# Kernel optimization log

Measured on AMD Instinct MI355X. Metric: run time of the kernel, lower is better.

Reference implementation:

```python
import jax, jax.numpy as jnp
import numpy as np

B, S, D, H, L = 16, 1024, 128, 8, 3
DFF = 4 * D  # 512
DH = D // H  # 16
NUM_CLASSES = 6


def layernorm(x, g, b, eps):
    mu = jnp.mean(x, axis=-1, keepdims=True)
    var = jnp.mean(jnp.square(x - mu), axis=-1, keepdims=True)
    return g * (x - mu) / jnp.sqrt(var + eps) + b


def setup_inputs() -> dict:
    key = jax.random.key(0)
    ks = jax.random.split(key, 16)
    sc = 0.05
    inp = {
        'x': jax.random.normal(ks[0], (B, S, D), dtype=jnp.float32),
        'Wq': jax.random.normal(ks[1], (L, D, D), dtype=jnp.float32) * sc,
        'bq': jnp.zeros((L, D), dtype=jnp.float32),
        'Wk': jax.random.normal(ks[2], (L, D, D), dtype=jnp.float32) * sc,
        'bk': jnp.zeros((L, D), dtype=jnp.float32),
        'Wv': jax.random.normal(ks[3], (L, D, D), dtype=jnp.float32) * sc,
        'bv': jnp.zeros((L, D), dtype=jnp.float32),
        'ln1_g': jnp.ones((L, D), dtype=jnp.float32),
        'ln1_b': jnp.zeros((L, D), dtype=jnp.float32),
        'W1': jax.random.normal(ks[4], (L, D, DFF), dtype=jnp.float32) * sc,
        'b1': jnp.zeros((L, DFF), dtype=jnp.float32),
        'W2': jax.random.normal(ks[5], (L, DFF, D), dtype=jnp.float32) * sc,
        'b2': jnp.zeros((L, D), dtype=jnp.float32),
        'ln2_g': jnp.ones((L, D), dtype=jnp.float32),
        'ln2_b': jnp.zeros((L, D), dtype=jnp.float32),
        'Wout': jax.random.normal(ks[6], (D, NUM_CLASSES), dtype=jnp.float32) * sc,
        'bout': jnp.zeros((NUM_CLASSES,), dtype=jnp.float32),
    }
    return inp


def reference(x, Wq, bq, Wk, bk, Wv, bv, ln1_g, ln1_b, W1, b1, W2, b2, ln2_g, ln2_b, Wout, bout):
    scale = 1.0 / jnp.sqrt(jnp.float32(DH))
    for l in range(L):
        # Q/K/V projections with ReLU activation (as in source Dense(..., relu))
        q = jax.nn.relu(jnp.einsum('bsd,de->bse', x, Wq[l]) + bq[l])
        k = jax.nn.relu(jnp.einsum('bsd,de->bse', x, Wk[l]) + bk[l])
        v = jax.nn.relu(jnp.einsum('bsd,de->bse', x, Wv[l]) + bv[l])
        # split-heads (tf.split axis=-1 / concat axis=0 == reshape to heads)
        qh = q.reshape(B, S, H, DH)
        kh = k.reshape(B, S, H, DH)
        vh = v.reshape(B, S, H, DH)
        scores = jnp.einsum('bqhd,bkhd->bhqk', qh, kh) * scale  # [B,H,S,S]
        attn = jax.nn.softmax(scores, axis=-1)
        o = jnp.einsum('bhqk,bkhd->bqhd', attn, vh).reshape(B, S, D)
        x = layernorm(o + x, ln1_g[l], ln1_b[l], 1e-8)
        # pointwise FFN (Conv1D kernel_size=1 == dense over last dim)
        h = jax.nn.relu(jnp.einsum('bsd,df->bsf', x, W1[l]) + b1[l])
        f = jnp.einsum('bsf,fd->bsd', h, W2[l]) + b2[l]
        x = layernorm(f + x, ln2_g[l], ln2_b[l], 1e-6)
    return jnp.einsum('bsd,dc->bsc', x, Wout) + bout
```

## Files before the change

kernel.cpp:

```cpp
#include <hip/hip_runtime.h>
#include <math.h>

#define Bq 16
#define Sq 1024
#define Dq 128
#define Hq 8
#define DHq 16
#define DFFq 512
#define Lq 3
#define NCLS 6
#define NROWS (Bq * Sq)
#define NX ((size_t)NROWS * Dq)

typedef __attribute__((ext_vector_type(8))) short    bf16x8;
typedef __attribute__((ext_vector_type(4))) float    f32x4;
typedef __attribute__((ext_vector_type(4))) _Float16 f16x4;
typedef __attribute__((ext_vector_type(8))) _Float16 f16x8;

__device__ inline ushort f32_to_bf16(float f) {
    union { float f; unsigned u; } v; v.f = f;
    unsigned r = v.u + 0x7fffu + ((v.u >> 16) & 1u);
    return (ushort)(r >> 16);
}

__global__ __launch_bounds__(256) void prep_kernel(
    const float* __restrict__ Wqp, const float* __restrict__ Wkp,
    const float* __restrict__ Wvp, const float* __restrict__ W1p,
    const float* __restrict__ W2p, const float* __restrict__ xp,
    ushort* __restrict__ wbf, ushort* __restrict__ xbf)
{
    const int gid = blockIdx.x * 256 + threadIdx.x;
    if (gid < 147456) {
        const int w   = gid / 49152;
        const int rem = gid - w * 49152;
        const int l   = rem >> 14;
        const int idx = rem & 16383;
        const int k   = idx >> 7;
        const int n   = idx & 127;
        const float* src = (w == 0) ? Wqp : (w == 1) ? Wkp : Wvp;
        const float scl = (w == 0) ? 0.25f : 1.0f;
        wbf[(size_t)(w * 3 + l) * 16384 + n * 128 + k] =
            f32_to_bf16(src[(size_t)l * 16384 + k * 128 + n] * scl);
    } else if (gid < 344064) {
        const int g   = gid - 147456;
        const int l   = g >> 16;
        const int idx = g & 65535;
        const int k   = idx >> 9;
        const int n   = idx & 511;
        wbf[147456 + (size_t)l * 65536 + n * 128 + k] =
            f32_to_bf16(W1p[(size_t)l * 65536 + k * 512 + n]);
    } else if (gid < 540672) {
        const int g   = gid - 344064;
        const int l   = g >> 16;
        const int idx = g & 65535;
        const int k   = idx >> 7;
        const int n   = idx & 127;
        wbf[344064 + (size_t)l * 65536 + n * 512 + k] =
            f32_to_bf16(W2p[(size_t)l * 65536 + k * 128 + n]);
    } else {
        const int g = gid - 540672;
        xbf[g] = f32_to_bf16(xp[g]);
    }
}

__global__ __launch_bounds__(256) void gemm_qkv(
    const ushort* __restrict__ A,
    const ushort* __restrict__ wq, const ushort* __restrict__ wk,
    const ushort* __restrict__ wv,
    const float* __restrict__ bqp, const float* __restrict__ bkp,
    const float* __restrict__ bvp,
    _Float16* __restrict__ qo, _Float16* __restrict__ ko,
    _Float16* __restrict__ vo)
{
    __shared__ ushort As[64 * 40];
    __shared__ ushort Bs[128 * 40];

    const int sel  = blockIdx.y;
    const ushort* Bt   = (sel == 0) ? wq : (sel == 1) ? wk : wv;
    const float*  bias = (sel == 0) ? bqp : (sel == 1) ? bkp : bvp;
    const float   bscl = (sel == 0) ? 0.25f : 1.0f;

    const int tid  = threadIdx.x;
    const int row0 = blockIdx.x * 64;
    const int wave = tid >> 6;
    const int lane = tid & 63;
    const int quad = lane >> 4;
    const int m16  = lane & 15;
    const int wm   = wave >> 1;
    const int wn   = wave & 1;

    const int sar = tid >> 2;
    const int sac = (tid & 3) * 8;

    f32x4 acc[2][4];
    #pragma unroll
    for (int i = 0; i < 2; ++i)
        #pragma unroll
        for (int j = 0; j < 4; ++j) acc[i][j] = (f32x4)0.f;

    for (int k0 = 0; k0 < 128; k0 += 32) {
        bf16x8 av = *(const bf16x8*)(A + (size_t)(row0 + sar) * 128 + k0 + sac);
        const int r1 = tid >> 2, r2 = r1 + 64;
        bf16x8 bv1 = *(const bf16x8*)(Bt + (size_t)r1 * 128 + k0 + sac);
        bf16x8 bv2 = *(const bf16x8*)(Bt + (size_t)r2 * 128 + k0 + sac);

        __syncthreads();
        *(bf16x8*)&As[sar * 40 + sac] = av;
        *(bf16x8*)&Bs[r1 * 40 + sac]  = bv1;
        *(bf16x8*)&Bs[r2 * 40 + sac]  = bv2;
        __syncthreads();

        bf16x8 af[2], bf[4];
        #pragma unroll
        for (int i = 0; i < 2; ++i)
            af[i] = *(const bf16x8*)&As[(32 * wm + 16 * i + m16) * 40 + quad * 8];
        #pragma unroll
        for (int j = 0; j < 4; ++j)
            bf[j] = *(const bf16x8*)&Bs[(64 * wn + 16 * j + m16) * 40 + quad * 8];
        #pragma unroll
        for (int i = 0; i < 2; ++i)
            #pragma unroll
            for (int j = 0; j < 4; ++j)
                acc[i][j] = __builtin_amdgcn_mfma_f32_16x16x32_bf16(af[i], bf[j], acc[i][j], 0, 0, 0);
    }

    #pragma unroll
    for (int i = 0; i < 2; ++i) {
        #pragma unroll
        for (int j = 0; j < 4; ++j) {
            const int col = 64 * wn + 16 * j + m16;
            const float bb = bias[col] * bscl;
            const int hh = col >> 4, dh = col & 15;
            #pragma unroll
            for (int r = 0; r < 4; ++r) {
                float val = fmaxf(acc[i][j][r] + bb, 0.f);
                const int gr = row0 + 32 * wm + 16 * i + quad * 4 + r;
                const int b = gr >> 10, s = gr & 1023;
                if (sel == 2) {
                    vo[(((size_t)b * Hq + hh) * DHq + dh) * Sq + s] = (_Float16)val;
                } else {
                    _Float16* outp = (sel == 0) ? qo : ko;
                    outp[(((size_t)b * Hq + hh) * Sq + s) * DHq + dh] = (_Float16)val;
                }
            }
        }
    }
}

__global__ __launch_bounds__(256) void gemm_ffn_fused(
    const float* __restrict__ o, const float* __restrict__ resid,
    const float* __restrict__ g1, const float* __restrict__ beta1,
    const ushort* __restrict__ W1t, const float* __restrict__ bias1,
    const ushort* __restrict__ W2t, const float* __restrict__ bias2,
    const float* __restrict__ g2, const float* __restrict__ beta2,
    float* __restrict__ xb, ushort* __restrict__ xbbf,
    const float* __restrict__ Wout, const float* __restrict__ bout,
    float* __restrict__ out, int last)
{
    __shared__ __align__(16) char smem[77696];
    ushort* Af   = (ushort*)smem;
    ushort* Hs   = (ushort*)(smem + 17408);
    ushort* Bs   = (ushort*)(smem + 50688);
    float*  wo_s = (float*)(smem + 50688);
    float*  vals = (float*)(smem + 60928);
    float*  mus  = (float*)(smem + 77440);
    float*  rsds = (float*)(smem + 77568);

    const int tid  = threadIdx.x;
    const int row0 = blockIdx.x * 32;
    const int wave = tid >> 6;
    const int lane = tid & 63;
    const int quad = lane >> 4;
    const int m16  = lane & 15;
    const int wm   = wave >> 1;
    const int wn   = wave & 1;
    const int sac  = (tid & 3) * 8;
    const int r1   = tid >> 2, r2 = r1 + 64;

    #pragma unroll 2
    for (int it = 0; it < 8; ++it) {
        const int rr = wave * 8 + it;
        const size_t base = (size_t)(row0 + rr) * Dq;
        float v0 = o[base + lane]      + resid[base + lane];
        float v1 = o[base + 64 + lane] + resid[base + 64 + lane];

        float s = v0 + v1;
        #pragma unroll
        for (int off = 32; off > 0; off >>= 1) s += __shfl_xor(s, off, 64);
        const float mu = s * (1.f / 128.f);
        const float d0 = v0 - mu, d1 = v1 - mu;
        float vs = d0 * d0 + d1 * d1;
        #pragma unroll
        for (int off = 32; off > 0; off >>= 1) vs += __shfl_xor(vs, off, 64);
        const float rstd = rsqrtf(vs * (1.f / 128.f) + 1e-8f);

        const float rv0 = g1[lane]      * d0 * rstd + beta1[lane];
        const float rv1 = g1[lane + 64] * d1 * rstd + beta1[lane + 64];
        Af[rr * 136 + lane]        = f32_to_bf16(rv0);
        Af[rr * 136 + 64 + lane]   = f32_to_bf16(rv1);
        vals[rr * 129 + lane]      = rv0;
        vals[rr * 129 + 64 + lane] = rv1;
    }

    for (int cc = 0; cc < 4; ++cc) {
        f32x4 acc[4];
        #pragma unroll
        for (int j = 0; j < 4; ++j) acc[j] = (f32x4)0.f;

        for (int k0 = 0; k0 < 128; k0 += 32) {
            bf16x8 bv1 = *(const bf16x8*)(W1t + (size_t)(cc * 128 + r1) * 128 + k0 + sac);
            bf16x8 bv2 = *(const bf16x8*)(W1t + (size_t)(cc * 128 + r2) * 128 + k0 + sac);

            __syncthreads();
            *(bf16x8*)&Bs[r1 * 40 + sac] = bv1;
            *(bf16x8*)&Bs[r2 * 40 + sac] = bv2;
            __syncthreads();

            const bf16x8 af = *(const bf16x8*)&Af[(16 * wm + m16) * 136 + k0 + quad * 8];
            bf16x8 bf[4];
            #pragma unroll
            for (int j = 0; j < 4; ++j)
                bf[j] = *(const bf16x8*)&Bs[(64 * wn + 16 * j + m16) * 40 + quad * 8];
            #pragma unroll
            for (int j = 0; j < 4; ++j)
                acc[j] = __builtin_amdgcn_mfma_f32_16x16x32_bf16(af, bf[j], acc[j], 0, 0, 0);
        }

        #pragma unroll
        for (int j = 0; j < 4; ++j) {
            const int col = cc * 128 + 64 * wn + 16 * j + m16;
            const float bb = bias1[col];
            #pragma unroll
            for (int r = 0; r < 4; ++r) {
                const int row = 16 * wm + quad * 4 + r;
                Hs[row * 520 + col] = f32_to_bf16(fmaxf(acc[j][r] + bb, 0.f));
            }
        }
    }

    f32x4 acc2[4];
    #pragma unroll
    for (int j = 0; j < 4; ++j) acc2[j] = (f32x4)0.f;

    for (int k0 = 0; k0 < DFFq; k0 += 32) {
        bf16x8 bv1 = *(const bf16x8*)(W2t + (size_t)r1 * DFFq + k0 + sac);
        bf16x8 bv2 = *(const bf16x8*)(W2t + (size_t)r2 * DFFq + k0 + sac);

        __syncthreads();
        *(bf16x8*)&Bs[r1 * 40 + sac] = bv1;
        *(bf16x8*)&Bs[r2 * 40 + sac] = bv2;
        __syncthreads();

        const bf16x8 af = *(const bf16x8*)&Hs[(16 * wm + m16) * 520 + k0 + quad * 8];
        bf16x8 bf[4];
        #pragma unroll
        for (int j = 0; j < 4; ++j)
            bf[j] = *(const bf16x8*)&Bs[(64 * wn + 16 * j + m16) * 40 + quad * 8];
        #pragma unroll
        for (int j = 0; j < 4; ++j)
            acc2[j] = __builtin_amdgcn_mfma_f32_16x16x32_bf16(af, bf[j], acc2[j], 0, 0, 0);
    }

    __syncthreads();

    float vreg[4][4];
    #pragma unroll
    for (int j = 0; j < 4; ++j) {
        const int col = 64 * wn + 16 * j + m16;
        const float bb = bias2[col];
        #pragma unroll
        for (int r = 0; r < 4; ++r) {
            const int row = 16 * wm + quad * 4 + r;
            float v = acc2[j][r] + bb + vals[row * 129 + col];
            vreg[j][r] = v;
            vals[row * 129 + col] = v;
        }
    }
    if (last) {
        #pragma unroll
        for (int i = 0; i < 3; ++i) wo_s[tid + i * 256] = Wout[tid + i * 256];
    }
    __syncthreads();

    if (tid < 32) {
        float s = 0.f, s2 = 0.f;
        #pragma unroll 8
        for (int c = 0; c < Dq; ++c) {
            float x = vals[tid * 129 + c];
            s += x; s2 = fmaf(x, x, s2);
        }
        const float mu  = s * (1.f / 128.f);
        const float var = s2 * (1.f / 128.f) - mu * mu;
        mus[tid]  = mu;
        rsds[tid] = rsqrtf(var + 1e-6f);
    }
    __syncthreads();

    if (!last) {
        #pragma unroll
        for (int j = 0; j < 4; ++j) {
            const int col = 64 * wn + 16 * j + m16;
            #pragma unroll
            for (int r = 0; r < 4; ++r) {
                const int row = 16 * wm + quad * 4 + r;
                const float rn = g2[col] * (vreg[j][r] - mus[row]) * rsds[row] + beta2[col];
                const size_t idx = (size_t)(row0 + row) * Dq + col;
                xb[idx]   = rn;
                xbbf[idx] = f32_to_bf16(rn);
            }
        }
    } else {
        #pragma unroll
        for (int j = 0; j < 4; ++j) {
            const int col = 64 * wn + 16 * j + m16;
            #pragma unroll
            for (int r = 0; r < 4; ++r) {
                const int row = 16 * wm + quad * 4 + r;
                vals[row * 129 + col] = g2[col] * (vreg[j][r] - mus[row]) * rsds[row] + beta2[col];
            }
        }
        __syncthreads();
        if (tid < 32 * NCLS) {
            const int row = tid / NCLS;
            const int c   = tid - row * NCLS;
            float a = bout[c];
            #pragma unroll 8
            for (int kk = 0; kk < Dq; ++kk)
                a = fmaf(vals[row * 129 + kk], wo_s[kk * NCLS + c], a);
            out[(size_t)(row0 + row) * NCLS + c] = a;
        }
    }
}

__global__ __launch_bounds__(256) void attn_mfma(
    const _Float16* __restrict__ q, const _Float16* __restrict__ k,
    const _Float16* __restrict__ vt, float* __restrict__ o)
{
    __shared__ _Float16 Ks[256 * 20];
    __shared__ _Float16 Vs[16 * 264];

    const int bh   = blockIdx.x;
    const int qc   = blockIdx.y;
    const int b    = bh >> 3;
    const int h    = bh & 7;
    const int tid  = threadIdx.x;
    const int wave = tid >> 6;
    const int lane = tid & 63;
    const int quad = lane >> 4;
    const int m16  = lane & 15;
    const int q0   = qc * 128 + wave * 32;

    const f16x4 qf0 = *(const f16x4*)(q + (((size_t)bh * Sq) + q0 + m16) * DHq + quad * 4);
    const f16x4 qf1 = *(const f16x4*)(q + (((size_t)bh * Sq) + q0 + 16 + m16) * DHq + quad * 4);

    const _Float16* kg  = k  + (size_t)bh * Sq * DHq;
    const _Float16* vtg = vt + (size_t)bh * DHq * Sq;

    f32x4 oacc0 = (f32x4)0.f, oacc1 = (f32x4)0.f;
    float lacc0 = 0.f, lacc1 = 0.f;

    const int krow = tid;
    const int vrow = tid >> 4;
    const int vcol = (tid & 15) * 16;

    for (int kb = 0; kb < 4; ++kb) {
        f16x8 ka  = *(const f16x8*)(kg + ((size_t)kb * 256 + krow) * DHq);
        f16x8 kb8 = *(const f16x8*)(kg + ((size_t)kb * 256 + krow) * DHq + 8);
        f16x8 va  = *(const f16x8*)(vtg + (size_t)vrow * Sq + kb * 256 + vcol);
        f16x8 vb  = *(const f16x8*)(vtg + (size_t)vrow * Sq + kb * 256 + vcol + 8);
        __syncthreads();
        *(f16x8*)&Ks[krow * 20 + 0] = ka;
        *(f16x8*)&Ks[krow * 20 + 8] = kb8;
        *(f16x8*)&Vs[vrow * 264 + vcol + 0] = va;
        *(f16x8*)&Vs[vrow * 264 + vcol + 8] = vb;
        __syncthreads();

        #pragma unroll 4
        for (int kt = 0; kt < 16; ++kt) {
            const f16x4 kf = *(const f16x4*)&Ks[(kt * 16 + m16) * 20 + quad * 4];
            const f16x4 vf = *(const f16x4*)&Vs[m16 * 264 + kt * 16 + quad * 4];

            f32x4 st0 = __builtin_amdgcn_mfma_f32_16x16x16f16(kf, qf0, (f32x4)0.f, 0, 0, 0);
            f32x4 st1 = __builtin_amdgcn_mfma_f32_16x16x16f16(kf, qf1, (f32x4)0.f, 0, 0, 0);

            float p00 = __expf(st0[0]);
            float p01 = __expf(st0[1]);
            float p02 = __expf(st0[2]);
            float p03 = __expf(st0[3]);
            float p10 = __expf(st1[0]);
            float p11 = __expf(st1[1]);
            float p12 = __expf(st1[2]);
            float p13 = __expf(st1[3]);
            lacc0 += (p00 + p01) + (p02 + p03);
            lacc1 += (p10 + p11) + (p12 + p13);

            f16x4 pf0, pf1;
            pf0[0] = (_Float16)p00; pf0[1] = (_Float16)p01;
            pf0[2] = (_Float16)p02; pf0[3] = (_Float16)p03;
            pf1[0] = (_Float16)p10; pf1[1] = (_Float16)p11;
            pf1[2] = (_Float16)p12; pf1[3] = (_Float16)p13;

            oacc0 = __builtin_amdgcn_mfma_f32_16x16x16f16(pf0, vf, oacc0, 0, 0, 0);
            oacc1 = __builtin_amdgcn_mfma_f32_16x16x16f16(pf1, vf, oacc1, 0, 0, 0);
        }
    }

    lacc0 += __shfl_xor(lacc0, 16, 64);
    lacc0 += __shfl_xor(lacc0, 32, 64);
    lacc1 += __shfl_xor(lacc1, 16, 64);
    lacc1 += __shfl_xor(lacc1, 32, 64);

    #pragma unroll
    for (int r = 0; r < 4; ++r) {
        const float ls0 = __shfl(lacc0, quad * 4 + r, 64);
        const float ls1 = __shfl(lacc1, quad * 4 + r, 64);
        o[((size_t)b * Sq + q0 + quad * 4 + r) * Dq + h * DHq + m16]      = oacc0[r] / ls0;
        o[((size_t)b * Sq + q0 + 16 + quad * 4 + r) * Dq + h * DHq + m16] = oacc1[r] / ls1;
    }
}

extern "C" void kernel_launch(void* const* d_in, const int* in_sizes, int n_in,
                              void* d_out, int out_size, void* d_ws, size_t ws_size,
                              hipStream_t stream)
{
    const float* x_in  = (const float*)d_in[0];
    const float* Wq    = (const float*)d_in[1];
    const float* bq    = (const float*)d_in[2];
    const float* Wk    = (const float*)d_in[3];
    const float* bk    = (const float*)d_in[4];
    const float* Wv    = (const float*)d_in[5];
    const float* bv    = (const float*)d_in[6];
    const float* ln1_g = (const float*)d_in[7];
    const float* ln1_b = (const float*)d_in[8];
    const float* W1    = (const float*)d_in[9];
    const float* b1    = (const float*)d_in[10];
    const float* W2    = (const float*)d_in[11];
    const float* b2    = (const float*)d_in[12];
    const float* ln2_g = (const float*)d_in[13];
    const float* ln2_b = (const float*)d_in[14];
    const float* Wout  = (const float*)d_in[15];
    const float* bout  = (const float*)d_in[16];
    float* out = (float*)d_out;

    float* ws = (float*)d_ws;
    _Float16* qf16 = (_Float16*)ws;
    _Float16* kf16 = (_Float16*)(ws + NX / 2);
    _Float16* vt16 = (_Float16*)(ws + NX);
    float*    xb   = ws + 9 * NX / 2;
    ushort*   xbf0 = (ushort*)(ws + 11 * NX / 2);
    ushort*   xbbf = (ushort*)(ws + 13 * NX / 2);
    ushort*   wbf  = (ushort*)(ws + 7 * NX);
    float*    obuf = ws + 8 * NX;

    prep_kernel<<<dim3(10304), dim3(256), 0, stream>>>(Wq, Wk, Wv, W1, W2, x_in, wbf, xbf0);

    const dim3 blk(256);
    const float* xcur = x_in;
    const ushort* xcur_bf = xbf0;

    for (int l = 0; l < Lq; ++l) {
        const ushort* wqt = wbf + (size_t)(0 * 3 + l) * 16384;
        const ushort* wkt = wbf + (size_t)(1 * 3 + l) * 16384;
        const ushort* wvt = wbf + (size_t)(2 * 3 + l) * 16384;
        const ushort* w1t = wbf + 147456 + (size_t)l * 65536;
        const ushort* w2t = wbf + 344064 + (size_t)l * 65536;

        gemm_qkv<<<dim3(256, 3), blk, 0, stream>>>(
            xcur_bf, wqt, wkt, wvt, bq + l * Dq, bk + l * Dq, bv + l * Dq,
            qf16, kf16, vt16);

        attn_mfma<<<dim3(Bq * Hq, 8), blk, 0, stream>>>(qf16, kf16, vt16, obuf);

        gemm_ffn_fused<<<dim3(512), blk, 0, stream>>>(
            obuf, xcur, ln1_g + l * Dq, ln1_b + l * Dq,
            w1t, b1 + l * DFFq, w2t, b2 + l * Dq,
            ln2_g + l * Dq, ln2_b + l * Dq,
            xb, xbbf, Wout, bout, out, (l == Lq - 1) ? 1 : 0);

        xcur = xb;
        xcur_bf = xbbf;
    }
}
```

Measured before the change: 278.8 us.

## Register-prefetch next tiles in GEMMs and attention; double queries per attention wave

```diff
diff --git a/kernel.cpp b/kernel.cpp
--- a/kernel.cpp
+++ b/kernel.cpp
@@ -91,6 +91,7 @@
 
     const int sar = tid >> 2;
     const int sac = (tid & 3) * 8;
+    const int r1  = tid >> 2, r2 = r1 + 64;
 
     f32x4 acc[2][4];
     #pragma unroll
@@ -98,17 +99,23 @@
         #pragma unroll
         for (int j = 0; j < 4; ++j) acc[i][j] = (f32x4)0.f;
 
-    for (int k0 = 0; k0 < 128; k0 += 32) {
-        bf16x8 av = *(const bf16x8*)(A + (size_t)(row0 + sar) * 128 + k0 + sac);
-        const int r1 = tid >> 2, r2 = r1 + 64;
-        bf16x8 bv1 = *(const bf16x8*)(Bt + (size_t)r1 * 128 + k0 + sac);
-        bf16x8 bv2 = *(const bf16x8*)(Bt + (size_t)r2 * 128 + k0 + sac);
-
+    bf16x8 av  = *(const bf16x8*)(A  + (size_t)(row0 + sar) * 128 + sac);
+    bf16x8 bv1 = *(const bf16x8*)(Bt + (size_t)r1 * 128 + sac);
+    bf16x8 bv2 = *(const bf16x8*)(Bt + (size_t)r2 * 128 + sac);
+
+    for (int kc = 0; kc < 4; ++kc) {
         __syncthreads();
         *(bf16x8*)&As[sar * 40 + sac] = av;
         *(bf16x8*)&Bs[r1 * 40 + sac]  = bv1;
         *(bf16x8*)&Bs[r2 * 40 + sac]  = bv2;
         __syncthreads();
+
+        if (kc < 3) {
+            const int k0 = (kc + 1) * 32;
+            av  = *(const bf16x8*)(A  + (size_t)(row0 + sar) * 128 + k0 + sac);
+            bv1 = *(const bf16x8*)(Bt + (size_t)r1 * 128 + k0 + sac);
+            bv2 = *(const bf16x8*)(Bt + (size_t)r2 * 128 + k0 + sac);
+        }
 
         bf16x8 af[2], bf[4];
         #pragma unroll
@@ -202,54 +209,74 @@
         vals[rr * 129 + 64 + lane] = rv1;
     }
 
-    for (int cc = 0; cc < 4; ++cc) {
-        f32x4 acc[4];
-        #pragma unroll
-        for (int j = 0; j < 4; ++j) acc[j] = (f32x4)0.f;
-
-        for (int k0 = 0; k0 < 128; k0 += 32) {
-            bf16x8 bv1 = *(const bf16x8*)(W1t + (size_t)(cc * 128 + r1) * 128 + k0 + sac);
-            bf16x8 bv2 = *(const bf16x8*)(W1t + (size_t)(cc * 128 + r2) * 128 + k0 + sac);
-
-            __syncthreads();
-            *(bf16x8*)&Bs[r1 * 40 + sac] = bv1;
-            *(bf16x8*)&Bs[r2 * 40 + sac] = bv2;
-            __syncthreads();
-
-            const bf16x8 af = *(const bf16x8*)&Af[(16 * wm + m16) * 136 + k0 + quad * 8];
-            bf16x8 bf[4];
+    bf16x8 pv1 = *(const bf16x8*)(W1t + (size_t)r1 * 128 + sac);
+    bf16x8 pv2 = *(const bf16x8*)(W1t + (size_t)r2 * 128 + sac);
+
+    f32x4 acc[4];
+    #pragma unroll
+    for (int j = 0; j < 4; ++j) acc[j] = (f32x4)0.f;
+
+    for (int idx = 0; idx < 16; ++idx) {
+        const int cc = idx >> 2;
+        const int k0 = (idx & 3) * 32;
+
+        __syncthreads();
+        *(bf16x8*)&Bs[r1 * 40 + sac] = pv1;
+        *(bf16x8*)&Bs[r2 * 40 + sac] = pv2;
+        __syncthreads();
+
+        if (idx < 15) {
+            const int n   = idx + 1;
+            const int ncc = n >> 2;
+            const int nk0 = (n & 3) * 32;
+            pv1 = *(const bf16x8*)(W1t + (size_t)(ncc * 128 + r1) * 128 + nk0 + sac);
+            pv2 = *(const bf16x8*)(W1t + (size_t)(ncc * 128 + r2) * 128 + nk0 + sac);
+        }
+
+        const bf16x8 af = *(const bf16x8*)&Af[(16 * wm + m16) * 136 + k0 + quad * 8];
+        bf16x8 bf[4];
+        #pragma unroll
+        for (int j = 0; j < 4; ++j)
+            bf[j] = *(const bf16x8*)&Bs[(64 * wn + 16 * j + m16) * 40 + quad * 8];
+        #pragma unroll
+        for (int j = 0; j < 4; ++j)
+            acc[j] = __builtin_amdgcn_mfma_f32_16x16x32_bf16(af, bf[j], acc[j], 0, 0, 0);
+
+        if ((idx & 3) == 3) {
             #pragma unroll
-            for (int j = 0; j < 4; ++j)
-                bf[j] = *(const bf16x8*)&Bs[(64 * wn + 16 * j + m16) * 40 + quad * 8];
-            #pragma unroll
-            for (int j = 0; j < 4; ++j)
-                acc[j] = __builtin_amdgcn_mfma_f32_16x16x32_bf16(af, bf[j], acc[j], 0, 0, 0);
-        }
-
-        #pragma unroll
-        for (int j = 0; j < 4; ++j) {
-            const int col = cc * 128 + 64 * wn + 16 * j + m16;
-            const float bb = bias1[col];
-            #pragma unroll
-            for (int r = 0; r < 4; ++r) {
-                const int row = 16 * wm + quad * 4 + r;
-                Hs[row * 520 + col] = f32_to_bf16(fmaxf(acc[j][r] + bb, 0.f));
+            for (int j = 0; j < 4; ++j) {
+                const int col = cc * 128 + 64 * wn + 16 * j + m16;
+                const float bb = bias1[col];
+                #pragma unroll
+                for (int r = 0; r < 4; ++r) {
+                    const int row = 16 * wm + quad * 4 + r;
+                    Hs[row * 520 + col] = f32_to_bf16(fmaxf(acc[j][r] + bb, 0.f));
+                }
+                acc[j] = (f32x4)0.f;
             }
         }
     }
 
+    bf16x8 qv1 = *(const bf16x8*)(W2t + (size_t)r1 * DFFq + sac);
+    bf16x8 qv2 = *(const bf16x8*)(W2t + (size_t)r2 * DFFq + sac);
+
     f32x4 acc2[4];
     #pragma unroll
     for (int j = 0; j < 4; ++j) acc2[j] = (f32x4)0.f;
 
-    for (int k0 = 0; k0 < DFFq; k0 += 32) {
-        bf16x8 bv1 = *(const bf16x8*)(W2t + (size_t)r1 * DFFq + k0 + sac);
-        bf16x8 bv2 = *(const bf16x8*)(W2t + (size_t)r2 * DFFq + k0 + sac);
-
-        __syncthreads();
-        *(bf16x8*)&Bs[r1 * 40 + sac] = bv1;
-        *(bf16x8*)&Bs[r2 * 40 + sac] = bv2;
-        __syncthreads();
+    for (int kc = 0; kc < 16; ++kc) {
+        const int k0 = kc * 32;
+
+        __syncthreads();
+        *(bf16x8*)&Bs[r1 * 40 + sac] = qv1;
+        *(bf16x8*)&Bs[r2 * 40 + sac] = qv2;
+        __syncthreads();
+
+        if (kc < 15) {
+            const int nk0 = (kc + 1) * 32;
+            qv1 = *(const bf16x8*)(W2t + (size_t)r1 * DFFq + nk0 + sac);
+            qv2 = *(const bf16x8*)(W2t + (size_t)r2 * DFFq + nk0 + sac);
+        }
 
         const bf16x8 af = *(const bf16x8*)&Hs[(16 * wm + m16) * 520 + k0 + quad * 8];
         bf16x8 bf[4];
@@ -348,26 +375,31 @@
     const int lane = tid & 63;
     const int quad = lane >> 4;
     const int m16  = lane & 15;
-    const int q0   = qc * 128 + wave * 32;
-
-    const f16x4 qf0 = *(const f16x4*)(q + (((size_t)bh * Sq) + q0 + m16) * DHq + quad * 4);
-    const f16x4 qf1 = *(const f16x4*)(q + (((size_t)bh * Sq) + q0 + 16 + m16) * DHq + quad * 4);
+    const int q0   = qc * 256 + wave * 64;
+
+    f16x4 qf[4];
+    #pragma unroll
+    for (int f = 0; f < 4; ++f)
+        qf[f] = *(const f16x4*)(q + (((size_t)bh * Sq) + q0 + f * 16 + m16) * DHq + quad * 4);
 
     const _Float16* kg  = k  + (size_t)bh * Sq * DHq;
     const _Float16* vtg = vt + (size_t)bh * DHq * Sq;
 
-    f32x4 oacc0 = (f32x4)0.f, oacc1 = (f32x4)0.f;
-    float lacc0 = 0.f, lacc1 = 0.f;
+    f32x4 oacc[4];
+    float lacc[4];
+    #pragma unroll
+    for (int f = 0; f < 4; ++f) { oacc[f] = (f32x4)0.f; lacc[f] = 0.f; }
 
     const int krow = tid;
     const int vrow = tid >> 4;
     const int vcol = (tid & 15) * 16;
 
+    f16x8 ka  = *(const f16x8*)(kg + (size_t)krow * DHq);
+    f16x8 kb8 = *(const f16x8*)(kg + (size_t)krow * DHq + 8);
+    f16x8 va  = *(const f16x8*)(vtg + (size_t)vrow * Sq + vcol);
+    f16x8 vb  = *(const f16x8*)(vtg + (size_t)vrow * Sq + vcol + 8);
+
     for (int kb = 0; kb < 4; ++kb) {
-        f16x8 ka  = *(const f16x8*)(kg + ((size_t)kb * 256 + krow) * DHq);
-        f16x8 kb8 = *(const f16x8*)(kg + ((size_t)kb * 256 + krow) * DHq + 8);
-        f16x8 va  = *(const f16x8*)(vtg + (size_t)vrow * Sq + kb * 256 + vcol);
-        f16x8 vb  = *(const f16x8*)(vtg + (size_t)vrow * Sq + kb * 256 + vcol + 8);
         __syncthreads();
         *(f16x8*)&Ks[krow * 20 + 0] = ka;
         *(f16x8*)&Ks[krow * 20 + 8] = kb8;
@@ -375,47 +407,48 @@
         *(f16x8*)&Vs[vrow * 264 + vcol + 8] = vb;
         __syncthreads();
 
-        #pragma unroll 4
+        if (kb < 3) {
+            const int nb = (kb + 1) * 256;
+            ka  = *(const f16x8*)(kg + ((size_t)nb + krow) * DHq);
+            kb8 = *(const f16x8*)(kg + ((size_t)nb + krow) * DHq + 8);
+            va  = *(const f16x8*)(vtg + (size_t)vrow * Sq + nb + vcol);
+            vb  = *(const f16x8*)(vtg + (size_t)vrow * Sq + nb + vcol + 8);
+        }
+
+        #pragma unroll 2
         for (int kt = 0; kt < 16; ++kt) {
             const f16x4 kf = *(const f16x4*)&Ks[(kt * 16 + m16) * 20 + quad * 4];
             const f16x4 vf = *(const f16x4*)&Vs[m16 * 264 + kt * 16 + quad * 4];
 
-            f32x4 st0 = __builtin_amdgcn_mfma_f32_16x16x16f16(kf, qf0, (f32x4)0.f, 0, 0, 0);
-            f32x4 st1 = __builtin_amdgcn_mfma_f32_16x16x16f16(kf, qf1, (f32x4)0.f, 0, 0, 0);
-
-            float p00 = __expf(st0[0]);
-            float p01 = __expf(st0[1]);
-            float p02 = __expf(st0[2]);
-            float p03 = __expf(st0[3]);
-            float p10 = __expf(st1[0]);
-            float p11 = __expf(st1[1]);
-            float p12 = __expf(st1[2]);
-            float p13 = __expf(st1[3]);
-            lacc0 += (p00 + p01) + (p02 + p03);
-            lacc1 += (p10 + p11) + (p12 + p13);
-
-            f16x4 pf0, pf1;
-            pf0[0] = (_Float16)p00; pf0[1] = (_Float16)p01;
-            pf0[2] = (_Float16)p02; pf0[3] = (_Float16)p03;
-            pf1[0] = (_Float16)p10; pf1[1] = (_Float16)p11;
-            pf1[2] = (_Float16)p12; pf1[3] = (_Float16)p13;
-
-            oacc0 = __builtin_amdgcn_mfma_f32_16x16x16f16(pf0, vf, oacc0, 0, 0, 0);
-            oacc1 = __builtin_amdgcn_mfma_f32_16x16x16f16(pf1, vf, oacc1, 0, 0, 0);
-        }
-    }
-
-    lacc0 += __shfl_xor(lacc0, 16, 64);
-    lacc0 += __shfl_xor(lacc0, 32, 64);
-    lacc1 += __shfl_xor(lacc1, 16, 64);
-    lacc1 += __shfl_xor(lacc1, 32, 64);
-
-    #pragma unroll
-    for (int r = 0; r < 4; ++r) {
-        const float ls0 = __shfl(lacc0, quad * 4 + r, 64);
-        const float ls1 = __shfl(lacc1, quad * 4 + r, 64);
-        o[((size_t)b * Sq + q0 + quad * 4 + r) * Dq + h * DHq + m16]      = oacc0[r] / ls0;
-        o[((size_t)b * Sq + q0 + 16 + quad * 4 + r) * Dq + h * DHq + m16] = oacc1[r] / ls1;
+            #pragma unroll
+            for (int f = 0; f < 4; ++f) {
+                f32x4 st = __builtin_amdgcn_mfma_f32_16x16x16f16(kf, qf[f], (f32x4)0.f, 0, 0, 0);
+                float p0 = __expf(st[0]);
+                float p1 = __expf(st[1]);
+                float p2 = __expf(st[2]);
+                float p3 = __expf(st[3]);
+                lacc[f] += (p0 + p1) + (p2 + p3);
+                f16x4 pf;
+                pf[0] = (_Float16)p0; pf[1] = (_Float16)p1;
+                pf[2] = (_Float16)p2; pf[3] = (_Float16)p3;
+                oacc[f] = __builtin_amdgcn_mfma_f32_16x16x16f16(pf, vf, oacc[f], 0, 0, 0);
+            }
+        }
+    }
+
+    #pragma unroll
+    for (int f = 0; f < 4; ++f) {
+        lacc[f] += __shfl_xor(lacc[f], 16, 64);
+        lacc[f] += __shfl_xor(lacc[f], 32, 64);
+    }
+
+    #pragma unroll
+    for (int f = 0; f < 4; ++f) {
+        #pragma unroll
+        for (int r = 0; r < 4; ++r) {
+            const float ls = __shfl(lacc[f], quad * 4 + r, 64);
+            o[((size_t)b * Sq + q0 + f * 16 + quad * 4 + r) * Dq + h * DHq + m16] = oacc[f][r] / ls;
+        }
     }
 }
 
@@ -469,7 +502,7 @@
             xcur_bf, wqt, wkt, wvt, bq + l * Dq, bk + l * Dq, bv + l * Dq,
             qf16, kf16, vt16);
 
-        attn_mfma<<<dim3(Bq * Hq, 8), blk, 0, stream>>>(qf16, kf16, vt16, obuf);
+        attn_mfma<<<dim3(Bq * Hq, 4), blk, 0, stream>>>(qf16, kf16, vt16, obuf);
 
         gemm_ffn_fused<<<dim3(512), blk, 0, stream>>>(
             obuf, xcur, ln1_g + l * Dq, ln1_b + l * Dq,
```

Result: slower. 287.1 us (+3.0%).

## Double FFN GEMM k-step per barrier and store residual staging in fp16

Applied to the files above, without the earlier changes.

```diff
diff --git a/kernel.cpp b/kernel.cpp
--- a/kernel.cpp
+++ b/kernel.cpp
@@ -157,14 +157,14 @@
     const float* __restrict__ Wout, const float* __restrict__ bout,
     float* __restrict__ out, int last)
 {
-    __shared__ __align__(16) char smem[77696];
-    ushort* Af   = (ushort*)smem;
-    ushort* Hs   = (ushort*)(smem + 17408);
-    ushort* Bs   = (ushort*)(smem + 50688);
-    float*  wo_s = (float*)(smem + 50688);
-    float*  vals = (float*)(smem + 60928);
-    float*  mus  = (float*)(smem + 77440);
-    float*  rsds = (float*)(smem + 77568);
+    __shared__ __align__(16) char smem[69120];
+    ushort*    Af   = (ushort*)smem;
+    ushort*    Hs   = (ushort*)(smem + 8704);
+    ushort*    Bs   = (ushort*)(smem + 41984);
+    float*     wo_s = (float*)(smem + 41984);
+    _Float16*  vals = (_Float16*)(smem + 60416);
+    float*     mus  = (float*)(smem + 68864);
+    float*     rsds = (float*)(smem + 68992);
 
     const int tid  = threadIdx.x;
     const int row0 = blockIdx.x * 32;
@@ -196,44 +196,56 @@
 
         const float rv0 = g1[lane]      * d0 * rstd + beta1[lane];
         const float rv1 = g1[lane + 64] * d1 * rstd + beta1[lane + 64];
-        Af[rr * 136 + lane]        = f32_to_bf16(rv0);
-        Af[rr * 136 + 64 + lane]   = f32_to_bf16(rv1);
-        vals[rr * 129 + lane]      = rv0;
-        vals[rr * 129 + 64 + lane] = rv1;
-    }
-
-    for (int cc = 0; cc < 4; ++cc) {
-        f32x4 acc[4];
-        #pragma unroll
-        for (int j = 0; j < 4; ++j) acc[j] = (f32x4)0.f;
-
-        for (int k0 = 0; k0 < 128; k0 += 32) {
-            bf16x8 bv1 = *(const bf16x8*)(W1t + (size_t)(cc * 128 + r1) * 128 + k0 + sac);
-            bf16x8 bv2 = *(const bf16x8*)(W1t + (size_t)(cc * 128 + r2) * 128 + k0 + sac);
-
-            __syncthreads();
-            *(bf16x8*)&Bs[r1 * 40 + sac] = bv1;
-            *(bf16x8*)&Bs[r2 * 40 + sac] = bv2;
-            __syncthreads();
-
-            const bf16x8 af = *(const bf16x8*)&Af[(16 * wm + m16) * 136 + k0 + quad * 8];
+        Af[rr * 136 + lane]       = f32_to_bf16(rv0);
+        Af[rr * 136 + 64 + lane]  = f32_to_bf16(rv1);
+        vals[rr * 132 + lane]     = (_Float16)rv0;
+        vals[rr * 132 + 64 + lane]= (_Float16)rv1;
+    }
+
+    f32x4 acc[4];
+    #pragma unroll
+    for (int j = 0; j < 4; ++j) acc[j] = (f32x4)0.f;
+
+    for (int idx = 0; idx < 8; ++idx) {
+        const int cc = idx >> 1;
+        const int k0 = (idx & 1) * 64;
+
+        bf16x8 w11 = *(const bf16x8*)(W1t + (size_t)(cc * 128 + r1) * 128 + k0 + sac);
+        bf16x8 w12 = *(const bf16x8*)(W1t + (size_t)(cc * 128 + r1) * 128 + k0 + 32 + sac);
+        bf16x8 w21 = *(const bf16x8*)(W1t + (size_t)(cc * 128 + r2) * 128 + k0 + sac);
+        bf16x8 w22 = *(const bf16x8*)(W1t + (size_t)(cc * 128 + r2) * 128 + k0 + 32 + sac);
+
+        __syncthreads();
+        *(bf16x8*)&Bs[r1 * 72 + sac]      = w11;
+        *(bf16x8*)&Bs[r1 * 72 + 32 + sac] = w12;
+        *(bf16x8*)&Bs[r2 * 72 + sac]      = w21;
+        *(bf16x8*)&Bs[r2 * 72 + 32 + sac] = w22;
+        __syncthreads();
+
+        #pragma unroll
+        for (int h = 0; h < 2; ++h) {
+            const int kk = k0 + h * 32;
+            const bf16x8 af = *(const bf16x8*)&Af[(16 * wm + m16) * 136 + kk + quad * 8];
             bf16x8 bf[4];
             #pragma unroll
             for (int j = 0; j < 4; ++j)
-                bf[j] = *(const bf16x8*)&Bs[(64 * wn + 16 * j + m16) * 40 + quad * 8];
+                bf[j] = *(const bf16x8*)&Bs[(64 * wn + 16 * j + m16) * 72 + h * 32 + quad * 8];
             #pragma unroll
             for (int j = 0; j < 4; ++j)
                 acc[j] = __builtin_amdgcn_mfma_f32_16x16x32_bf16(af, bf[j], acc[j], 0, 0, 0);
         }
 
-        #pragma unroll
-        for (int j = 0; j < 4; ++j) {
-            const int col = cc * 128 + 64 * wn + 16 * j + m16;
-            const float bb = bias1[col];
-            #pragma unroll
-            for (int r = 0; r < 4; ++r) {
-                const int row = 16 * wm + quad * 4 + r;
-                Hs[row * 520 + col] = f32_to_bf16(fmaxf(acc[j][r] + bb, 0.f));
+        if (idx & 1) {
+            #pragma unroll
+            for (int j = 0; j < 4; ++j) {
+                const int col = cc * 128 + 64 * wn + 16 * j + m16;
+                const float bb = bias1[col];
+                #pragma unroll
+                for (int r = 0; r < 4; ++r) {
+                    const int row = 16 * wm + quad * 4 + r;
+                    Hs[row * 520 + col] = f32_to_bf16(fmaxf(acc[j][r] + bb, 0.f));
+                }
+                acc[j] = (f32x4)0.f;
             }
         }
     }
@@ -242,23 +254,33 @@
     #pragma unroll
     for (int j = 0; j < 4; ++j) acc2[j] = (f32x4)0.f;
 
-    for (int k0 = 0; k0 < DFFq; k0 += 32) {
-        bf16x8 bv1 = *(const bf16x8*)(W2t + (size_t)r1 * DFFq + k0 + sac);
-        bf16x8 bv2 = *(const bf16x8*)(W2t + (size_t)r2 * DFFq + k0 + sac);
-
-        __syncthreads();
-        *(bf16x8*)&Bs[r1 * 40 + sac] = bv1;
-        *(bf16x8*)&Bs[r2 * 40 + sac] = bv2;
-        __syncthreads();
-
-        const bf16x8 af = *(const bf16x8*)&Hs[(16 * wm + m16) * 520 + k0 + quad * 8];
-        bf16x8 bf[4];
-        #pragma unroll
-        for (int j = 0; j < 4; ++j)
-            bf[j] = *(const bf16x8*)&Bs[(64 * wn + 16 * j + m16) * 40 + quad * 8];
-        #pragma unroll
-        for (int j = 0; j < 4; ++j)
-            acc2[j] = __builtin_amdgcn_mfma_f32_16x16x32_bf16(af, bf[j], acc2[j], 0, 0, 0);
+    for (int kc = 0; kc < 8; ++kc) {
+        const int k0 = kc * 64;
+
+        bf16x8 w11 = *(const bf16x8*)(W2t + (size_t)r1 * DFFq + k0 + sac);
+        bf16x8 w12 = *(const bf16x8*)(W2t + (size_t)r1 * DFFq + k0 + 32 + sac);
+        bf16x8 w21 = *(const bf16x8*)(W2t + (size_t)r2 * DFFq + k0 + sac);
+        bf16x8 w22 = *(const bf16x8*)(W2t + (size_t)r2 * DFFq + k0 + 32 + sac);
+
+        __syncthreads();
+        *(bf16x8*)&Bs[r1 * 72 + sac]      = w11;
+        *(bf16x8*)&Bs[r1 * 72 + 32 + sac] = w12;
+        *(bf16x8*)&Bs[r2 * 72 + sac]      = w21;
+        *(bf16x8*)&Bs[r2 * 72 + 32 + sac] = w22;
+        __syncthreads();
+
+        #pragma unroll
+        for (int h = 0; h < 2; ++h) {
+            const int kk = k0 + h * 32;
+            const bf16x8 af = *(const bf16x8*)&Hs[(16 * wm + m16) * 520 + kk + quad * 8];
+            bf16x8 bf[4];
+            #pragma unroll
+            for (int j = 0; j < 4; ++j)
+                bf[j] = *(const bf16x8*)&Bs[(64 * wn + 16 * j + m16) * 72 + h * 32 + quad * 8];
+            #pragma unroll
+            for (int j = 0; j < 4; ++j)
+                acc2[j] = __builtin_amdgcn_mfma_f32_16x16x32_bf16(af, bf[j], acc2[j], 0, 0, 0);
+        }
     }
 
     __syncthreads();
@@ -271,9 +293,9 @@
         #pragma unroll
         for (int r = 0; r < 4; ++r) {
             const int row = 16 * wm + quad * 4 + r;
-            float v = acc2[j][r] + bb + vals[row * 129 + col];
+            float v = acc2[j][r] + bb + (float)vals[row * 132 + col];
             vreg[j][r] = v;
-            vals[row * 129 + col] = v;
+            vals[row * 132 + col] = (_Float16)v;
         }
     }
     if (last) {
@@ -286,7 +308,7 @@
         float s = 0.f, s2 = 0.f;
         #pragma unroll 8
         for (int c = 0; c < Dq; ++c) {
-            float x = vals[tid * 129 + c];
+            float x = (float)vals[tid * 132 + c];
             s += x; s2 = fmaf(x, x, s2);
         }
         const float mu  = s * (1.f / 128.f);
@@ -316,7 +338,8 @@
             #pragma unroll
             for (int r = 0; r < 4; ++r) {
                 const int row = 16 * wm + quad * 4 + r;
-                vals[row * 129 + col] = g2[col] * (vreg[j][r] - mus[row]) * rsds[row] + beta2[col];
+                vals[row * 132 + col] =
+                    (_Float16)(g2[col] * (vreg[j][r] - mus[row]) * rsds[row] + beta2[col]);
             }
         }
         __syncthreads();
@@ -326,7 +349,7 @@
             float a = bout[c];
             #pragma unroll 8
             for (int kk = 0; kk < Dq; ++kk)
-                a = fmaf(vals[row * 129 + kk], wo_s[kk * NCLS + c], a);
+                a = fmaf((float)vals[row * 132 + kk], wo_s[kk * NCLS + c], a);
             out[(size_t)(row0 + row) * NCLS + c] = a;
         }
     }
```

Measured after the change: 275.9 us. No clear change (-1.0%).
